# Performance work log

Measured on AMD Instinct MI355X. Metric: run time of the kernel, lower is better.

Reference implementation:

```python
import jax, jax.numpy as jnp
import numpy as np

B, N, C = 128, 36, 1024
K_NB = 16            # neighbors per node (top-k, includes loop)
KERNEL = 8           # number of Gaussian kernels
OUT = 1024           # out_dim; per-kernel out = OUT // KERNEL
PI = np.float32(np.pi)


def setup_inputs() -> dict:
    key = jax.random.key(0)
    ks = jax.random.split(key, 9)
    node_feats = jax.random.normal(ks[0], (B, N, C), dtype=jnp.float32)
    node_centre = jax.random.uniform(ks[1], (B, N, 2), dtype=jnp.float32)
    neighbor_idx = jax.random.randint(ks[2], (B * N, K_NB), 0, B * N, dtype=jnp.int32)
    graph_weights = jax.random.uniform(ks[3], (B * N * K_NB, 1), dtype=jnp.float32)
    # Gaussian kernel params (per reset_parameters)
    mean_rho = jax.random.uniform(ks[4], (1, KERNEL), dtype=jnp.float32)
    mean_theta = jax.random.uniform(ks[5], (1, KERNEL), minval=-PI, maxval=PI, dtype=jnp.float32)
    precision_rho = jax.random.uniform(ks[6], (1, KERNEL), minval=0.5, maxval=1.0, dtype=jnp.float32)
    precision_theta = jax.random.uniform(ks[7], (1, KERNEL), minval=0.5, maxval=1.0, dtype=jnp.float32)
    # per-kernel Linear(node_dim, out_dim//kernel, bias=False), stacked: [K, d_out_k, C]
    conv_w = jax.random.normal(ks[8], (KERNEL, OUT // KERNEL, C), dtype=jnp.float32) * (1.0 / np.sqrt(C))
    return {
        "node_feats": node_feats,
        "node_centre": node_centre,
        "neighbor_idx": neighbor_idx,
        "graph_weights": graph_weights,
        "mean_rho": mean_rho,
        "mean_theta": mean_theta,
        "precision_rho": precision_rho,
        "precision_theta": precision_theta,
        "conv_w": conv_w,
    }


def _forward(node_feats, node_centre, graph_weights,
             mean_rho, mean_theta, precision_rho, precision_theta,
             conv_w, neighbor_idx):
    b, n, c = node_feats.shape
    bn = b * n
    # pseudo polar coordinates per edge: centre_i - centre_j
    centre = node_centre.reshape(bn, 2)                       # [BN, 2]
    diff = centre[:, None, :] - centre[neighbor_idx]          # [BN, K_nb, 2]
    coord_x = diff[..., 0].reshape(-1)                        # [E]
    coord_y = diff[..., 1].reshape(-1)
    rho = jnp.sqrt(coord_x ** 2 + coord_y ** 2)
    theta = jnp.arctan2(coord_x, coord_y)
    # Gaussian mixture membership weights over KERNEL kernels
    w_rho = jnp.exp(-0.5 * (rho[:, None] - mean_rho) ** 2 / (1e-14 + precision_rho ** 2))
    first_angle = jnp.abs(theta[:, None] - mean_theta)
    second_angle = jnp.abs(2.0 * PI - first_angle)
    w_theta = jnp.exp(-0.5 * jnp.minimum(first_angle, second_angle) ** 2 / (1e-14 + precision_theta ** 2))
    weights = w_rho * w_theta                                  # [E, KERNEL]
    weights = jnp.where(jnp.isnan(weights), 0.0, weights)
    weights = weights / jnp.sum(weights, axis=1, keepdims=True)
    # combine with graph edge weights
    edge_w = graph_weights * weights                           # [E, KERNEL]
    edge_w = edge_w.reshape(bn, K_NB, KERNEL).transpose(0, 2, 1)  # [BN, K, K_nb]
    # gather neighbor features and weighted aggregate (bmm)
    nbr = node_feats.reshape(bn, c)[neighbor_idx]              # [BN, K_nb, C]
    agg = jnp.einsum('ekn,enc->ekc', edge_w, nbr)              # [BN, KERNEL, C]
    agg = agg.reshape(b, n, KERNEL, c)
    # per-kernel linear then concat over kernel dim
    out = jnp.einsum('bnkc,kdc->bnkd', agg, conv_w)            # [B, N, KERNEL, OUT//KERNEL]
    out = out.reshape(b, n, -1)                                # [B, N, OUT]
    return jax.nn.relu(out)


def reference(node_feats, node_centre, neighbor_idx, graph_weights,
              mean_rho, mean_theta, precision_rho, precision_theta, conv_w):
    return _forward(node_feats, node_centre, graph_weights,
                    mean_rho, mean_theta, precision_rho, precision_theta,
                    conv_w, neighbor_idx)
```

## Files before the change

### kernel.cpp

```cpp
#include <hip/hip_runtime.h>
#include <hip/hip_bf16.h>
#include <stdint.h>

#define B_DIM   128
#define N_DIM   36
#define C_DIM   1024
#define KNB     16
#define NKER    8
#define OUTD    1024
#define BN_NODES (B_DIM * N_DIM)
#define E_EDGES  (BN_NODES * KNB)
#define PI_F 3.14159265358979323846f

#define TM 128
#define TN 128
#define BK 64
#define KIT (C_DIM / BK)
#define CLP 136

typedef __attribute__((ext_vector_type(8))) short bf16x8;
typedef __attribute__((ext_vector_type(4))) float floatx4;

struct alignas(8) U16x4 { unsigned short x, y, z, w; };

__device__ __forceinline__ unsigned short f2bf(float f) {
  union { float f; uint32_t u; } v; v.f = f;
  uint32_t u = v.u;
  return (unsigned short)((u + 0x7fffu + ((u >> 16) & 1u)) >> 16);
}
__device__ __forceinline__ float bf2f(unsigned short h) {
  union { uint32_t u; float f; } v; v.u = ((uint32_t)h) << 16;
  return v.f;
}

__device__ __forceinline__ void gload16(const void* g, void* l) {
  __builtin_amdgcn_global_load_lds((__attribute__((address_space(1))) void*)(g),
                                   (__attribute__((address_space(3))) void*)(l),
                                   16, 0, 0);
}

__global__ __launch_bounds__(256)
void cast_kernel(const float* __restrict__ feats,
                 const float* __restrict__ cw,
                 unsigned short* __restrict__ fb,
                 unsigned short* __restrict__ wb)
{
  const int NF4 = (BN_NODES * C_DIM) / 4;
  const int NW4 = (C_DIM * OUTD) / 4;
  int tid = blockIdx.x * 256 + threadIdx.x;
  if (tid < NF4) {
    float4 v = ((const float4*)feats)[tid];
    U16x4 o = { f2bf(v.x), f2bf(v.y), f2bf(v.z), f2bf(v.w) };
    ((U16x4*)fb)[tid] = o;
  } else {
    int t = tid - NF4;
    if (t < NW4) {
      float4 v = ((const float4*)cw)[t];
      U16x4 o = { f2bf(v.x), f2bf(v.y), f2bf(v.z), f2bf(v.w) };
      ((U16x4*)wb)[t] = o;
    }
  }
}

__global__ __launch_bounds__(256)
void gemm_bt(const unsigned short* __restrict__ A,
             const unsigned short* __restrict__ Bt,
             unsigned short* __restrict__ D)
{
  __shared__ unsigned short smem[4 * TM * BK];

  const int tid  = threadIdx.x;
  const int lane = tid & 63;
  const int wave = tid >> 6;
  const int wr   = wave >> 1;
  const int wc   = wave & 1;
  const int row0 = blockIdx.x * TM;
  const int col0 = blockIdx.y * TN;

  const int q  = lane >> 4;
  const int lr = lane & 15;

  floatx4 acc[4][4] = {};

  int offA[4], offB[4];
#pragma unroll
  for (int i = 0; i < 4; ++i) {
    int c   = tid + 256 * i;
    int row = c >> 3, qc = c & 7;
    int sw  = qc ^ (row & 7);
    offA[i] = (row0 + row) * C_DIM + sw * 8;
    offB[i] = (col0 + row) * C_DIM + sw * 8;
  }

#define DMA(T, P) do {                                                       \
    _Pragma("unroll") for (int i = 0; i < 4; ++i) {                          \
      gload16(A  + offA[i] + (T) * BK,                                       \
              &smem[(P) * TM * BK + (tid + 256 * i) * 8]);                   \
      gload16(Bt + offB[i] + (T) * BK,                                       \
              &smem[(2 + (P)) * TM * BK + (tid + 256 * i) * 8]);             \
    }                                                                        \
  } while (0)

  DMA(0, 0);

  for (int t = 0; t < KIT; ++t) {
    const int p = t & 1;
    __syncthreads();
    if (t + 1 < KIT) DMA(t + 1, 1 - p);

    const int aBase = p * TM * BK;
    const int bBase = (2 + p) * TM * BK;
#pragma unroll
    for (int kc = 0; kc < 2; ++kc) {
      const int sc = ((kc * 4 + q) ^ (lr & 7)) * 8;
      bf16x8 af[4], bfr[4];
#pragma unroll
      for (int i = 0; i < 4; ++i) {
        af[i]  = *(const bf16x8*)&smem[aBase + (wr * 64 + i * 16 + lr) * BK + sc];
        bfr[i] = *(const bf16x8*)&smem[bBase + (wc * 64 + i * 16 + lr) * BK + sc];
      }
#pragma unroll
      for (int i = 0; i < 4; ++i)
#pragma unroll
        for (int j = 0; j < 4; ++j)
          acc[i][j] = __builtin_amdgcn_mfma_f32_16x16x32_bf16(
              af[i], bfr[j], acc[i][j], 0, 0, 0);
    }
  }
#undef DMA

  __syncthreads();
#pragma unroll
  for (int i = 0; i < 4; ++i)
#pragma unroll
    for (int j = 0; j < 4; ++j)
#pragma unroll
      for (int r = 0; r < 4; ++r)
        smem[(wr * 64 + i * 16 + q * 4 + r) * CLP + wc * 64 + j * 16 + lr] =
            f2bf(acc[i][j][r]);
  __syncthreads();
#pragma unroll
  for (int i = 0; i < 8; ++i) {
    int c = tid + 256 * i;
    int row = c >> 4, qc = c & 15;
    *(uint4*)&D[(size_t)(row0 + row) * OUTD + col0 + qc * 8] =
        *(const uint4*)&smem[row * CLP + qc * 8];
  }
}

__global__ __launch_bounds__(256)
void agg_fused(const unsigned short* __restrict__ proj,
               const float* __restrict__ centre,
               const int*   __restrict__ nbr,
               const float* __restrict__ gw,
               const float* __restrict__ mrho,
               const float* __restrict__ mth,
               const float* __restrict__ prho,
               const float* __restrict__ pth,
               float* __restrict__ out)
{
  __shared__ int   idx[KNB];
  __shared__ float nx[KNB], ny[KNB];
  __shared__ float cc[2];
  __shared__ float wk[KNB][NKER];
  __shared__ float scl[KNB];
  __shared__ float ew[NKER][KNB];

  const int n = blockIdx.x;
  const int t = threadIdx.x;

  if (t < KNB) {
    int m = nbr[n * KNB + t];
    idx[t] = m;
    nx[t] = centre[2 * m];
    ny[t] = centre[2 * m + 1];
  } else if (t == KNB) {
    cc[0] = centre[2 * n];
    cc[1] = centre[2 * n + 1];
  }
  __syncthreads();

  if (t < 128) {
    int j = t >> 3, k = t & 7;
    float cx = cc[0] - nx[j];
    float cy = cc[1] - ny[j];
    float rho   = sqrtf(cx * cx + cy * cy);
    float theta = atan2f(cx, cy);
    float dr = rho - mrho[k];
    float pr = prho[k];
    float w_r = expf(-0.5f * dr * dr / (1e-14f + pr * pr));
    float fa = fabsf(theta - mth[k]);
    float sa = fabsf(2.0f * PI_F - fa);
    float mm = fminf(fa, sa);
    float pt = pth[k];
    float w_t = expf(-0.5f * mm * mm / (1e-14f + pt * pt));
    float ww = w_r * w_t;
    wk[j][k] = (ww != ww) ? 0.f : ww;
  }
  __syncthreads();

  if (t < KNB) {
    float s = 0.f;
#pragma unroll
    for (int k = 0; k < NKER; ++k) s += wk[t][k];
    scl[t] = gw[n * KNB + t] / s;
  }
  __syncthreads();

  if (t < 128) {
    int j = t >> 3, k = t & 7;
    ew[k][j] = wk[j][k] * scl[j];
  }
  __syncthreads();

  const int k = t >> 5;
  float a0 = 0.f, a1 = 0.f, a2 = 0.f, a3 = 0.f;
#pragma unroll
  for (int j = 0; j < KNB; ++j) {
    float wv = ew[k][j];
    U16x4 v = *(const U16x4*)&proj[(size_t)idx[j] * OUTD + t * 4];
    a0 += wv * bf2f(v.x);
    a1 += wv * bf2f(v.y);
    a2 += wv * bf2f(v.z);
    a3 += wv * bf2f(v.w);
  }
  float4 r;
  r.x = fmaxf(a0, 0.f); r.y = fmaxf(a1, 0.f);
  r.z = fmaxf(a2, 0.f); r.w = fmaxf(a3, 0.f);
  ((float4*)out)[(size_t)n * (OUTD / 4) + t] = r;
}

extern "C" void kernel_launch(void* const* d_in, const int* in_sizes, int n_in,
                              void* d_out, int out_size, void* d_ws, size_t ws_size,
                              hipStream_t stream)
{
  const float* feats  = (const float*)d_in[0];
  const float* centre = (const float*)d_in[1];
  const int*   nbr    = (const int*)  d_in[2];
  const float* gw     = (const float*)d_in[3];
  const float* mrho   = (const float*)d_in[4];
  const float* mth    = (const float*)d_in[5];
  const float* prho   = (const float*)d_in[6];
  const float* pth    = (const float*)d_in[7];
  const float* cw     = (const float*)d_in[8];
  float* out = (float*)d_out;

  char* ws = (char*)d_ws;
  unsigned short* fb   = (unsigned short*)(ws);
  unsigned short* wb   = (unsigned short*)(ws + 9437184);
  unsigned short* proj = (unsigned short*)(ws + 11534336);

  cast_kernel<<<dim3(((BN_NODES * C_DIM) / 4 + (C_DIM * OUTD) / 4) / 256),
                dim3(256), 0, stream>>>(feats, cw, fb, wb);
  gemm_bt<<<dim3(BN_NODES / TM, OUTD / TN), dim3(256), 0, stream>>>(fb, wb, proj);
  agg_fused<<<dim3(BN_NODES), dim3(256), 0, stream>>>(
      proj, centre, nbr, gw, mrho, mth, prho, pth, out);
}
```

Baseline: 126.0 us.

## Shrink GEMM M-tile to 64 and process two nodes per aggregation block

The projection GEMM tile drops from 128x128 to 64x128, doubling the grid from 288 to 576 blocks so more CUs are busy on the 4608x1024 output, with smaller LDS and register use per block. The aggregation kernel now handles two nodes per 256-thread block. Each thread loads 8 bf16 values with a 16-byte load instead of 4, and all threads stay active in the weight computation. The cost is lower operand reuse per GEMM block (more B-tile reloads) and more per-thread register work in the aggregation.

After: 121.7 us, median of 2. -3.4%, faster.

```diff
diff --git a/kernel.cpp b/kernel.cpp
--- a/kernel.cpp
+++ b/kernel.cpp
@@ -12,11 +12,13 @@
 #define E_EDGES  (BN_NODES * KNB)
 #define PI_F 3.14159265358979323846f
 
-#define TM 128
+#define TM 64
 #define TN 128
 #define BK 64
 #define KIT (C_DIM / BK)
 #define CLP 136
+#define A_OFF(p) ((p) * TM * BK)
+#define B_OFF(p) (2 * TM * BK + (p) * TN * BK)
 
 typedef __attribute__((ext_vector_type(8))) short bf16x8;
 typedef __attribute__((ext_vector_type(4))) float floatx4;
@@ -28,8 +30,12 @@
   uint32_t u = v.u;
   return (unsigned short)((u + 0x7fffu + ((u >> 16) & 1u)) >> 16);
 }
-__device__ __forceinline__ float bf2f(unsigned short h) {
-  union { uint32_t u; float f; } v; v.u = ((uint32_t)h) << 16;
+__device__ __forceinline__ float bf2f_lo(uint32_t pair) {
+  union { uint32_t u; float f; } v; v.u = pair << 16;
+  return v.f;
+}
+__device__ __forceinline__ float bf2f_hi(uint32_t pair) {
+  union { uint32_t u; float f; } v; v.u = pair & 0xffff0000u;
   return v.f;
 }
 
@@ -67,38 +73,40 @@
              const unsigned short* __restrict__ Bt,
              unsigned short* __restrict__ D)
 {
-  __shared__ unsigned short smem[4 * TM * BK];
+  __shared__ unsigned short smem[2 * TM * BK + 2 * TN * BK];
 
   const int tid  = threadIdx.x;
   const int lane = tid & 63;
   const int wave = tid >> 6;
-  const int wr   = wave >> 1;
-  const int wc   = wave & 1;
+  const int wm   = wave >> 1;
+  const int wn   = wave & 1;
   const int row0 = blockIdx.x * TM;
   const int col0 = blockIdx.y * TN;
 
   const int q  = lane >> 4;
   const int lr = lane & 15;
 
-  floatx4 acc[4][4] = {};
-
-  int offA[4], offB[4];
+  floatx4 acc[2][4] = {};
+
+  int offA[2], offB[4];
+#pragma unroll
+  for (int i = 0; i < 2; ++i) {
+    int c = tid + 256 * i, row = c >> 3, qc = c & 7;
+    offA[i] = (row0 + row) * C_DIM + (qc ^ (row & 7)) * 8;
+  }
 #pragma unroll
   for (int i = 0; i < 4; ++i) {
-    int c   = tid + 256 * i;
-    int row = c >> 3, qc = c & 7;
-    int sw  = qc ^ (row & 7);
-    offA[i] = (row0 + row) * C_DIM + sw * 8;
-    offB[i] = (col0 + row) * C_DIM + sw * 8;
+    int c = tid + 256 * i, row = c >> 3, qc = c & 7;
+    offB[i] = (col0 + row) * C_DIM + (qc ^ (row & 7)) * 8;
   }
 
 #define DMA(T, P) do {                                                       \
-    _Pragma("unroll") for (int i = 0; i < 4; ++i) {                          \
-      gload16(A  + offA[i] + (T) * BK,                                       \
-              &smem[(P) * TM * BK + (tid + 256 * i) * 8]);                   \
+    _Pragma("unroll") for (int i = 0; i < 2; ++i)                            \
+      gload16(A + offA[i] + (T) * BK,                                        \
+              &smem[A_OFF(P) + (tid + 256 * i) * 8]);                        \
+    _Pragma("unroll") for (int i = 0; i < 4; ++i)                            \
       gload16(Bt + offB[i] + (T) * BK,                                       \
-              &smem[(2 + (P)) * TM * BK + (tid + 256 * i) * 8]);             \
-    }                                                                        \
+              &smem[B_OFF(P) + (tid + 256 * i) * 8]);                        \
   } while (0)
 
   DMA(0, 0);
@@ -108,19 +116,20 @@
     __syncthreads();
     if (t + 1 < KIT) DMA(t + 1, 1 - p);
 
-    const int aBase = p * TM * BK;
-    const int bBase = (2 + p) * TM * BK;
+    const int aBase = A_OFF(p);
+    const int bBase = B_OFF(p);
 #pragma unroll
     for (int kc = 0; kc < 2; ++kc) {
       const int sc = ((kc * 4 + q) ^ (lr & 7)) * 8;
-      bf16x8 af[4], bfr[4];
-#pragma unroll
-      for (int i = 0; i < 4; ++i) {
-        af[i]  = *(const bf16x8*)&smem[aBase + (wr * 64 + i * 16 + lr) * BK + sc];
-        bfr[i] = *(const bf16x8*)&smem[bBase + (wc * 64 + i * 16 + lr) * BK + sc];
-      }
-#pragma unroll
-      for (int i = 0; i < 4; ++i)
+      bf16x8 af[2], bfr[4];
+#pragma unroll
+      for (int i = 0; i < 2; ++i)
+        af[i]  = *(const bf16x8*)&smem[aBase + (wm * 32 + i * 16 + lr) * BK + sc];
+#pragma unroll
+      for (int j = 0; j < 4; ++j)
+        bfr[j] = *(const bf16x8*)&smem[bBase + (wn * 64 + j * 16 + lr) * BK + sc];
+#pragma unroll
+      for (int i = 0; i < 2; ++i)
 #pragma unroll
         for (int j = 0; j < 4; ++j)
           acc[i][j] = __builtin_amdgcn_mfma_f32_16x16x32_bf16(
@@ -131,16 +140,16 @@
 
   __syncthreads();
 #pragma unroll
-  for (int i = 0; i < 4; ++i)
+  for (int i = 0; i < 2; ++i)
 #pragma unroll
     for (int j = 0; j < 4; ++j)
 #pragma unroll
       for (int r = 0; r < 4; ++r)
-        smem[(wr * 64 + i * 16 + q * 4 + r) * CLP + wc * 64 + j * 16 + lr] =
+        smem[(wm * 32 + i * 16 + q * 4 + r) * CLP + wn * 64 + j * 16 + lr] =
             f2bf(acc[i][j][r]);
   __syncthreads();
 #pragma unroll
-  for (int i = 0; i < 8; ++i) {
+  for (int i = 0; i < 4; ++i) {
     int c = tid + 256 * i;
     int row = c >> 4, qc = c & 15;
     *(uint4*)&D[(size_t)(row0 + row) * OUTD + col0 + qc * 8] =
@@ -159,31 +168,35 @@
                const float* __restrict__ pth,
                float* __restrict__ out)
 {
-  __shared__ int   idx[KNB];
-  __shared__ float nx[KNB], ny[KNB];
-  __shared__ float cc[2];
-  __shared__ float wk[KNB][NKER];
-  __shared__ float scl[KNB];
-  __shared__ float ew[NKER][KNB];
-
-  const int n = blockIdx.x;
-  const int t = threadIdx.x;
-
-  if (t < KNB) {
-    int m = nbr[n * KNB + t];
-    idx[t] = m;
-    nx[t] = centre[2 * m];
-    ny[t] = centre[2 * m + 1];
-  } else if (t == KNB) {
-    cc[0] = centre[2 * n];
-    cc[1] = centre[2 * n + 1];
-  }
-  __syncthreads();
-
-  if (t < 128) {
-    int j = t >> 3, k = t & 7;
-    float cx = cc[0] - nx[j];
-    float cy = cc[1] - ny[j];
+  __shared__ int   idx[2][KNB];
+  __shared__ float nxy[2][KNB][2];
+  __shared__ float cxy[2][2];
+  __shared__ float wk[2][KNB][NKER];
+  __shared__ float scl[2][KNB];
+  __shared__ float ew[2][NKER][KNB];
+
+  const int n0   = blockIdx.x * 2;
+  const int t    = threadIdx.x;
+  const int half = t >> 7;
+  const int u    = t & 127;
+
+  if (t < 32) {
+    int h = t >> 4, j = t & 15;
+    int m = nbr[(n0 + h) * KNB + j];
+    idx[h][j] = m;
+    nxy[h][j][0] = centre[2 * m];
+    nxy[h][j][1] = centre[2 * m + 1];
+  } else if (t < 34) {
+    int h = t - 32;
+    cxy[h][0] = centre[2 * (n0 + h)];
+    cxy[h][1] = centre[2 * (n0 + h) + 1];
+  }
+  __syncthreads();
+
+  {
+    int j = u >> 3, k = u & 7;
+    float cx = cxy[half][0] - nxy[half][j][0];
+    float cy = cxy[half][1] - nxy[half][j][1];
     float rho   = sqrtf(cx * cx + cy * cy);
     float theta = atan2f(cx, cy);
     float dr = rho - mrho[k];
@@ -195,39 +208,44 @@
     float pt = pth[k];
     float w_t = expf(-0.5f * mm * mm / (1e-14f + pt * pt));
     float ww = w_r * w_t;
-    wk[j][k] = (ww != ww) ? 0.f : ww;
-  }
-  __syncthreads();
-
-  if (t < KNB) {
+    wk[half][j][k] = (ww != ww) ? 0.f : ww;
+  }
+  __syncthreads();
+
+  if (u < KNB) {
     float s = 0.f;
 #pragma unroll
-    for (int k = 0; k < NKER; ++k) s += wk[t][k];
-    scl[t] = gw[n * KNB + t] / s;
-  }
-  __syncthreads();
-
-  if (t < 128) {
-    int j = t >> 3, k = t & 7;
-    ew[k][j] = wk[j][k] * scl[j];
-  }
-  __syncthreads();
-
-  const int k = t >> 5;
-  float a0 = 0.f, a1 = 0.f, a2 = 0.f, a3 = 0.f;
+    for (int k = 0; k < NKER; ++k) s += wk[half][u][k];
+    scl[half][u] = gw[(n0 + half) * KNB + u] / s;
+  }
+  __syncthreads();
+
+  {
+    int j = u >> 3, k = u & 7;
+    ew[half][k][j] = wk[half][j][k] * scl[half][j];
+  }
+  __syncthreads();
+
+  const int n = n0 + half;
+  const int k = u >> 4;
+  float a[8] = {0.f, 0.f, 0.f, 0.f, 0.f, 0.f, 0.f, 0.f};
 #pragma unroll
   for (int j = 0; j < KNB; ++j) {
-    float wv = ew[k][j];
-    U16x4 v = *(const U16x4*)&proj[(size_t)idx[j] * OUTD + t * 4];
-    a0 += wv * bf2f(v.x);
-    a1 += wv * bf2f(v.y);
-    a2 += wv * bf2f(v.z);
-    a3 += wv * bf2f(v.w);
-  }
-  float4 r;
-  r.x = fmaxf(a0, 0.f); r.y = fmaxf(a1, 0.f);
-  r.z = fmaxf(a2, 0.f); r.w = fmaxf(a3, 0.f);
-  ((float4*)out)[(size_t)n * (OUTD / 4) + t] = r;
+    float wv = ew[half][k][j];
+    uint4 v = *(const uint4*)&proj[(size_t)idx[half][j] * OUTD + u * 8];
+    a[0] += wv * bf2f_lo(v.x);  a[1] += wv * bf2f_hi(v.x);
+    a[2] += wv * bf2f_lo(v.y);  a[3] += wv * bf2f_hi(v.y);
+    a[4] += wv * bf2f_lo(v.z);  a[5] += wv * bf2f_hi(v.z);
+    a[6] += wv * bf2f_lo(v.w);  a[7] += wv * bf2f_hi(v.w);
+  }
+  float4 r0, r1;
+  r0.x = fmaxf(a[0], 0.f); r0.y = fmaxf(a[1], 0.f);
+  r0.z = fmaxf(a[2], 0.f); r0.w = fmaxf(a[3], 0.f);
+  r1.x = fmaxf(a[4], 0.f); r1.y = fmaxf(a[5], 0.f);
+  r1.z = fmaxf(a[6], 0.f); r1.w = fmaxf(a[7], 0.f);
+  float* o = out + (size_t)n * OUTD + u * 8;
+  *(float4*)(o)     = r0;
+  *(float4*)(o + 4) = r1;
 }
 
 extern "C" void kernel_launch(void* const* d_in, const int* in_sizes, int n_in,
@@ -253,6 +271,6 @@
   cast_kernel<<<dim3(((BN_NODES * C_DIM) / 4 + (C_DIM * OUTD) / 4) / 256),
                 dim3(256), 0, stream>>>(feats, cw, fb, wb);
   gemm_bt<<<dim3(BN_NODES / TM, OUTD / TN), dim3(256), 0, stream>>>(fb, wb, proj);
-  agg_fused<<<dim3(BN_NODES), dim3(256), 0, stream>>>(
+  agg_fused<<<dim3(BN_NODES / 2), dim3(256), 0, stream>>>(
       proj, centre, nbr, gw, mrho, mth, prho, pth, out);
 }
```
